# Kernel optimization log

Measured on AMD Instinct MI355X. Metric: run time of the kernel, lower is better.

Reference implementation:

```python
import jax, jax.numpy as jnp
import numpy as np

N, T = 128, 256
QN, QD = 16, 32           # Qn_num, Qn_dim
QL_SIZES = [100] * 8      # Ql category sizes
LD = 32                   # Ql_dim
H = 1024                  # hidden_dim
L = 2                     # layer_num
OUT = 2                   # output_dim
IN_DIM = QN * QD + len(QL_SIZES) * LD  # 768
EPS = 1e-5


def setup_inputs() -> dict:
    key = jax.random.key(0)
    ks = jax.random.split(key, 14)
    qn = jax.random.normal(ks[0], (N, T, QN), dtype=jnp.float32)
    ql = jax.random.randint(ks[1], (N, T, len(QL_SIZES)), 0, 100).astype(jnp.float32)
    x = jnp.concatenate([qn, ql], axis=2)  # [N,T,24]
    std = 1.0 / np.sqrt(H)
    u = lambda k, s: jax.random.uniform(k, s, minval=-std, maxval=std, dtype=jnp.float32)
    return dict(
        x=x,
        QnV=jax.random.normal(ks[2], (QN, QD), dtype=jnp.float32) * 0.5,
        QlV=jax.random.normal(ks[3], (sum(QL_SIZES), LD), dtype=jnp.float32) * 0.5,
        bn_gamma=jnp.ones((QN,), jnp.float32),
        bn_beta=jnp.zeros((QN,), jnp.float32),
        W0=u(ks[4], (IN_DIM + H, 4 * H)), b0=u(ks[5], (4 * H,)),
        W1=u(ks[6], (2 * H, 4 * H)), b1=u(ks[7], (4 * H,)),
        ln_gamma=u(ks[8], (L, 4, H)), ln_beta=u(ks[9], (L, 4, H)),
        fcW=u(ks[10], (H, OUT)), fcb=u(ks[11], (OUT,)),
    )


def _layernorm(v, g, b):
    m = v.mean(-1, keepdims=True)
    s = v.var(-1, keepdims=True)
    return (v - m) * jax.lax.rsqrt(s + EPS) * g + b


def reference(x, QnV, QlV, bn_gamma, bn_beta, W0, b0, W1, b1, ln_gamma, ln_beta, fcW, fcb):
    # ---- data_trans ----
    qn = x[:, :, :QN]                               # [N,T,QN] float features
    ql_idx = x[:, :, QN:].astype(jnp.int32)         # [N,T,Lq] category indices
    offsets = jnp.asarray(np.concatenate([[0], np.cumsum(QL_SIZES)[:-1]]), jnp.int32)
    ql_idx = ql_idx + offsets.reshape(1, 1, -1)
    # BatchNorm1d (training mode): stats over flattened N*T rows, per feature
    flat = qn.reshape(-1, QN)
    mu = flat.mean(0)
    var = flat.var(0)
    qn = (qn - mu) * jax.lax.rsqrt(var + EPS) * bn_gamma + bn_beta
    qn_emb = qn[..., None] * QnV                    # einsum ijk,kd->ijkd : [N,T,QN,QD]
    ql_emb = QlV[ql_idx]                            # [N,T,Lq,LD]
    feats = jnp.concatenate([qn_emb, ql_emb], axis=2).reshape(N, T, IN_DIM)

    Ws, bs = [W0, W1], [b0, b1]

    def step(carry, xt):  # xt: [N, IN_DIM]
        hn, cn = carry     # each [L, N, H]
        xcur = xt
        hs, cs = [], []
        for i in range(L):
            inp = jnp.concatenate([hn[i], xcur], axis=1)
            gates = inp @ Ws[i] + bs[i]             # [N, 4H]
            ig, fg, gg, og = jnp.split(gates, 4, axis=1)
            ig = jax.nn.sigmoid(_layernorm(ig, ln_gamma[i, 0], ln_beta[i, 0]))
            fg = jax.nn.sigmoid(_layernorm(fg, ln_gamma[i, 1], ln_beta[i, 1]))
            gn = _layernorm(gg, ln_gamma[i, 2], ln_beta[i, 2])
            og = jax.nn.sigmoid(_layernorm(og, ln_gamma[i, 3], ln_beta[i, 3]))
            c = cn[i] * fg + ig * jnp.tanh(gn)
            # NOTE: original adds the pre-tanh normalized cellgate (quirk, kept faithful)
            xcur = og * jnp.tanh(c) + gn
            hs.append(xcur)
            cs.append(c)
        return (jnp.stack(hs), jnp.stack(cs)), xcur  # emit last layer h

    h0 = jnp.zeros((L, N, H), jnp.float32)
    c0 = jnp.zeros((L, N, H), jnp.float32)
    xs = jnp.transpose(feats, (1, 0, 2))            # [T, N, IN_DIM]
    _, outs = jax.lax.scan(step, (h0, c0), xs)      # [T, N, H]
    outs = jnp.transpose(outs, (1, 0, 2))           # [N, T, H]
    logits = outs @ fcW + fcb                       # [N, T, OUT]
    return jax.nn.softmax(logits, axis=2)
```

## Files before the change

kernel.cpp:

```cpp
#include <hip/hip_runtime.h>
#include <math.h>


#define N_   128
#define T_   256
#define QN_  16
#define INX  24
#define H_   1024
#define G4   4096
#define FDIM 768
#define EPS_ 1e-5f
#define K0_  1792
#define K1_  2048
#define NSLOT 8
#define HSZ  ((size_t)N_ * H_)
#define SSLOT 16
#define SLSZ (512 * 16)

typedef unsigned short u16;
typedef unsigned int u32;
typedef unsigned long long u64;
typedef __attribute__((ext_vector_type(8))) short bf16x8;
typedef __attribute__((ext_vector_type(4))) float f32x4;

__device__ __forceinline__ float sigmoidf_(float v) { return 1.0f / (1.0f + expf(-v)); }

__device__ __forceinline__ u16 f2bf(float f) {
  unsigned u = __float_as_uint(f);
  u += 0x7fffu + ((u >> 16) & 1u);
  return (u16)(u >> 16);
}
__device__ __forceinline__ float bf2f(u16 x) {
  return __uint_as_float((u32)x << 16);
}

__device__ __forceinline__ void st_u64g(void* p, u64 v) {
  __hip_atomic_store((u64*)p, v, __ATOMIC_RELAXED, __HIP_MEMORY_SCOPE_AGENT);
}
__device__ __forceinline__ void st_f32g(float* p, float v) {
  __hip_atomic_store(p, v, __ATOMIC_RELAXED, __HIP_MEMORY_SCOPE_AGENT);
}
__device__ __forceinline__ u64 ld_u64g(const void* p) {
  return __hip_atomic_load((const u64*)p, __ATOMIC_RELAXED, __HIP_MEMORY_SCOPE_AGENT);
}
__device__ __forceinline__ void atomAdd_(float* p, float v) {
  __hip_atomic_fetch_add(p, v, __ATOMIC_RELAXED, __HIP_MEMORY_SCOPE_AGENT);
}

__global__ __launch_bounds__(256) void bn_stats_k(const float* __restrict__ x,
    const float* __restrict__ gamma, const float* __restrict__ beta,
    float* __restrict__ scale, float* __restrict__ shift) {
  int q = blockIdx.x;
  int tid = threadIdx.x;
  float s = 0.f, s2 = 0.f;
  for (int r = tid; r < N_ * T_; r += 256) {
    float v = x[(size_t)r * INX + q];
    s += v; s2 += v * v;
  }
  for (int off = 32; off; off >>= 1) { s += __shfl_down(s, off); s2 += __shfl_down(s2, off); }
  __shared__ float red[2][4];
  int w = tid >> 6;
  if ((tid & 63) == 0) { red[0][w] = s; red[1][w] = s2; }
  __syncthreads();
  if (tid == 0) {
    float S = 0.f, S2 = 0.f;
    for (int i = 0; i < 4; ++i) { S += red[0][i]; S2 += red[1][i]; }
    float m   = S  / (float)(N_ * T_);
    float var = S2 / (float)(N_ * T_) - m * m;
    float rs  = rsqrtf(var + EPS_);
    scale[q] = rs * gamma[q];
    shift[q] = beta[q] - m * rs * gamma[q];
  }
}

__global__ __launch_bounds__(256) void feats_all_k(const float* __restrict__ x,
    const float* __restrict__ scale, const float* __restrict__ shift,
    const float* __restrict__ QnV, const float* __restrict__ QlV,
    u16* __restrict__ ft) {
  int rid = blockIdx.x;
  int t = rid >> 7, n = rid & 127;
  const float* xr = x + ((size_t)n * T_ + t) * INX;
  u16* frow = ft + (size_t)rid * FDIM;
  for (int f = threadIdx.x; f < FDIM; f += 256) {
    int d = f & 31;
    float v;
    if (f < 512) {
      int q = f >> 5;
      v = (xr[q] * scale[q] + shift[q]) * QnV[q * 32 + d];
    } else {
      int cg_ = (f - 512) >> 5;
      int idx = (int)xr[QN_ + cg_] + cg_ * 100;
      v = QlV[idx * 32 + d];
    }
    frow[f] = f2bf(v);
  }
}

__global__ __launch_bounds__(256) void wconv_k(const float* __restrict__ W,
                                               u16* __restrict__ WtP, int K) {
  __shared__ u16 L[64][72];
  int tid = threadIdx.x;
  int k0 = blockIdx.x * 64, n0 = blockIdx.y * 64;
#pragma unroll
  for (int it = 0; it < 16; ++it) {
    int e = it * 256 + tid;
    int r = e >> 6, c = e & 63;
    L[r][c] = f2bf(W[(size_t)(k0 + r) * G4 + n0 + c]);
  }
  __syncthreads();
  int n = tid >> 2, ks = (tid & 3) << 4;
  int col = n0 + n;
  int b = (col & 1023) >> 3;
  int j = (col >> 10) * 8 + (col & 7);
  u16* dst = WtP + ((size_t)(b * 32 + j)) * K + k0 + ks;
#pragma unroll
  for (int jj = 0; jj < 16; ++jj) dst[jj] = L[ks + jj][n];
}

__device__ __forceinline__ void arrive_(u32* cnts, int fam, int sub) {
  __hip_atomic_fetch_add(&cnts[(fam * 8 + sub) * 16], 1u,
                         __ATOMIC_RELAXED, __HIP_MEMORY_SCOPE_AGENT);
}
__device__ __forceinline__ void poll_(u32* cnts, int fam, int sub, u32 tgt) {
  while (__hip_atomic_load(&cnts[(fam * 8 + sub) * 16],
                           __ATOMIC_RELAXED, __HIP_MEMORY_SCOPE_AGENT) < tgt)
    __builtin_amdgcn_s_sleep(1);
}
__device__ __forceinline__ void acqf_(int tid) {
  if (tid < 64) __builtin_amdgcn_fence(__ATOMIC_ACQUIRE, "agent");
  __syncthreads();
}

template<int NS>
__device__ __forceinline__ void gpart(f32x4& a0, f32x4& a1,
    const u16* __restrict__ abase, const u16* __restrict__ wb0,
    const u16* __restrict__ wb1, int cb, int swz, int g) {
#pragma unroll 8
  for (int kc = 0; kc < NS; ++kc) {
    bf16x8 av = *(const bf16x8*)(abase + kc * 32);
    int c = ((cb + kc * 4 + g) ^ swz) << 3;
    bf16x8 bv0 = *(const bf16x8*)(wb0 + c);
    bf16x8 bv1 = *(const bf16x8*)(wb1 + c);
    a0 = __builtin_amdgcn_mfma_f32_16x16x32_bf16(av, bv0, a0, 0, 0, 0);
    a1 = __builtin_amdgcn_mfma_f32_16x16x32_bf16(av, bv1, a1, 0, 0, 0);
  }
}

__device__ __forceinline__ float lnrm(float v, u64 sq, float g_, float b_) {
  float s = __uint_as_float((u32)sq);
  float q = __uint_as_float((u32)(sq >> 32));
  float mean = s * (1.f / (float)H_);
  float var  = q * (1.f / (float)H_) - mean * mean;
  return (v - mean) * rsqrtf(var + EPS_) * g_ + b_;
}

__global__ __launch_bounds__(512, 2) void persist_k(
    const u16* __restrict__ WtP0, const u16* __restrict__ WtP1,
    const u16* __restrict__ ft,
    u16* __restrict__ h0s, u16* __restrict__ h1s,
    const float* __restrict__ b0, const float* __restrict__ b1,
    const float* __restrict__ lng, const float* __restrict__ lnb,
    const float* __restrict__ fcW, const float* __restrict__ fcb,
    float* __restrict__ statsA, float* __restrict__ statsB,
    u32* __restrict__ cnts, float* __restrict__ out) {
  __shared__ u16 wlds[32 * K1_];
  const int bcu = blockIdx.x, tid = threadIdx.x;
  const int isL0 = bcu < 128;
  const int b    = isL0 ? bcu : bcu - 128;
  const int wave = tid >> 6, lane = tid & 63;
  const int vcol = lane & 15, g4 = lane >> 4;
  const int ga = vcol >> 3, hh = vcol & 7;
  const int swz = vcol & 7;
  const int rowA  = wave * 16 + vcol;
  const int wbase = wave * 16;
  const int sub   = b >> 4;
  const int hbase = b * 8;
  const int K = isL0 ? K0_ : K1_;

  {
    const u16* wsrc = isL0 ? WtP0 + (size_t)b * 32 * K0_
                           : WtP1 + (size_t)b * 32 * K1_;
    int kc8 = K >> 3;
    for (int cid = tid; cid < 32 * kc8; cid += 512) {
      int j = cid / kc8, ck = cid - j * kc8;
      *(bf16x8*)&wlds[j * K + ((ck ^ (j & 7)) << 3)] =
          *(const bf16x8*)&wsrc[(size_t)j * K + (ck << 3)];
    }
  }
  __syncthreads();
  acqf_(tid);

  const u16* wb0p = &wlds[vcol * K];
  const u16* wb1p = &wlds[(vcol + 16) * K];

  const float* bW   = isL0 ? b0 : b1;
  const float* lngW = isL0 ? lng : lng + 4 * H_;
  const float* lnbW = isL0 ? lnb : lnb + 4 * H_;
  const int colA = ga * H_ + hbase + hh;
  const int colB = (ga + 2) * H_ + hbase + hh;
  const float bias0v = bW[colA], bias1v = bW[colB];
  const float lng0v = lngW[colA], lnb0v = lnbW[colA];
  const float lng1v = lngW[colB], lnb1v = lnbW[colB];
  const float fcb0 = fcb[0], fcb1 = fcb[1];

  float cst[4] = {0.f, 0.f, 0.f, 0.f};

  if (isL0) {
    f32x4 acN0 = {0.f, 0.f, 0.f, 0.f}, acN1 = acN0;
    gpart<24>(acN0, acN1, ft + (size_t)rowA * FDIM + g4 * 8, wb0p, wb1p, 128, swz, g4);

    for (int t = 0; t < T_; ++t) {
      const u32 tgt = (u32)(t + 1) * 16u;
      u16* h0w = h0s + (size_t)(t & (NSLOT - 1)) * HSZ;
      const u16* h0r = h0s + (size_t)((t - 1) & (NSLOT - 1)) * HSZ;
      float* stA = statsA + (size_t)(t & (SSLOT - 1)) * SLSZ;

      f32x4 ac0 = acN0, ac1 = acN1;
      gpart<32>(ac0, ac1, h0r + (size_t)rowA * H_ + g4 * 8, wb0p, wb1p, 0, swz, g4);
      f32x4 accb0, accb1;
#pragma unroll
      for (int r = 0; r < 4; ++r) { accb0[r] = ac0[r] + bias0v; accb1[r] = ac1[r] + bias1v; }

#pragma unroll
      for (int r = 0; r < 4; ++r) {
        int row = wbase + g4 * 4 + r;
        float s0 = accb0[r], q0 = s0 * s0, s1 = accb1[r], q1 = s1 * s1;
#pragma unroll
        for (int off = 1; off <= 4; off <<= 1) {
          s0 += __shfl_xor(s0, off); q0 += __shfl_xor(q0, off);
          s1 += __shfl_xor(s1, off); q1 += __shfl_xor(q1, off);
        }
        if (hh == 0) {
          atomAdd_(&stA[(row * 4 + ga) * 16],     s0);
          atomAdd_(&stA[(row * 4 + ga) * 16 + 1], q0);
          atomAdd_(&stA[(row * 4 + ga + 2) * 16],     s1);
          atomAdd_(&stA[(row * 4 + ga + 2) * 16 + 1], q1);
        }
      }
      asm volatile("s_waitcnt vmcnt(0)" ::: "memory");
      __syncthreads();
      if (tid == 0) arrive_(cnts, 0, sub);

      {
        float* zs = statsA + (size_t)((t + 8) & (SSLOT - 1)) * SLSZ;
        if (tid < 64) st_f32g(&zs[(b * 4 + (tid >> 4)) * 16 + (tid & 15)], 0.f);
        int tn = (t + 1 < T_) ? t + 1 : t;
        acN0[0] = 0.f; acN0[1] = 0.f; acN0[2] = 0.f; acN0[3] = 0.f;
        acN1 = acN0;
        gpart<24>(acN0, acN1, ft + ((size_t)tn * N_ + rowA) * FDIM + g4 * 8,
                  wb0p, wb1p, 128, swz, g4);
      }
      if (tid < 8) poll_(cnts, 0, tid, tgt);
      else if (tid < 16 && t >= 7) poll_(cnts, 2, tid - 8, (u32)(t - 6) * 16u);
      __syncthreads();

      u64 sv0[4], sv1[4];
#pragma unroll
      for (int r = 0; r < 4; ++r) {
        int row = wbase + g4 * 4 + r;
        sv0[r] = ld_u64g(&stA[(row * 4 + ga) * 16]);
        sv1[r] = ld_u64g(&stA[(row * 4 + ga + 2) * 16]);
      }
#pragma unroll
      for (int r = 0; r < 4; ++r) {
        int row = wbase + g4 * 4 + r;
        float nv0 = lnrm(accb0[r], sv0[r], lng0v, lnb0v);
        float nv1 = lnrm(accb1[r], sv1[r], lng1v, lnb1v);
        float o0 = __shfl_xor(nv0, 8), o1 = __shfl_xor(nv1, 8);
        float vi = ga ? o0 : nv0;
        float vf = ga ? nv0 : o0;
        float vg = ga ? o1 : nv1;
        float vo = ga ? nv1 : o1;
        float igt = sigmoidf_(vi), fgt = sigmoidf_(vf), ogt = sigmoidf_(vo);
        float cn = cst[r] * fgt + igt * tanhf(vg);
        float xn = ogt * tanhf(cn) + vg;
        cst[r] = cn;
        u32 xv = f2bf(xn);
        u32 oth = __shfl_xor((int)xv, 1);
        u32 pr = (hh & 1) ? ((oth & 0xffffu) | (xv << 16)) : ((xv & 0xffffu) | (oth << 16));
        u32 p2 = __shfl_xor((int)pr, 2);
        if (ga == 0 && (hh & 3) == 0)
          st_u64g(&h0w[(size_t)row * H_ + hbase + hh], ((u64)p2 << 32) | pr);
      }
      asm volatile("s_waitcnt vmcnt(0)" ::: "memory");
      __syncthreads();
      if (tid == 0) arrive_(cnts, 1, sub);
      if (tid < 8) poll_(cnts, 1, tid, tgt);
      __syncthreads();
      if ((t & (NSLOT - 1)) == NSLOT - 2) acqf_(tid);
    }
  } else {
    for (int t = 0; t < T_; ++t) {
      const u32 tgt = (u32)(t + 1) * 16u;
      const u16* h0r = h0s + (size_t)(t & (NSLOT - 1)) * HSZ;
      u16* h1w = h1s + (size_t)(t & (NSLOT - 1)) * HSZ;
      const u16* h1r = h1s + (size_t)((t - 1) & (NSLOT - 1)) * HSZ;
      float* stA = statsB + (size_t)(t & (SSLOT - 1)) * SLSZ;

      if (t > 0 && wave == 0) {
        const u16* hrow = h1r + (size_t)b * H_;
        int col = lane * 16;
        bf16x8 v0 = *(const bf16x8*)(hrow + col);
        bf16x8 v1 = *(const bf16x8*)(hrow + col + 8);
        float L0v = 0.f, L1v = 0.f;
#pragma unroll
        for (int j = 0; j < 8; ++j) {
          float x0 = bf2f((u16)v0[j]);
          float2 fw = *(const float2*)&fcW[(col + j) * 2];
          L0v = fmaf(x0, fw.x, L0v); L1v = fmaf(x0, fw.y, L1v);
          float x1 = bf2f((u16)v1[j]);
          float2 fw2 = *(const float2*)&fcW[(col + 8 + j) * 2];
          L0v = fmaf(x1, fw2.x, L0v); L1v = fmaf(x1, fw2.y, L1v);
        }
#pragma unroll
        for (int off = 1; off <= 32; off <<= 1) { L0v += __shfl_xor(L0v, off); L1v += __shfl_xor(L1v, off); }
        if (lane == 0) {
          L0v += fcb0; L1v += fcb1;
          float mx = fmaxf(L0v, L1v);
          float e0 = expf(L0v - mx), e1 = expf(L1v - mx);
          float inv = 1.f / (e0 + e1);
          *(float2*)&out[((size_t)b * T_ + (t - 1)) * 2] = make_float2(e0 * inv, e1 * inv);
        }
      }

      f32x4 ac0 = {0.f, 0.f, 0.f, 0.f}, ac1 = ac0;
      gpart<32>(ac0, ac1, h1r + (size_t)rowA * H_ + g4 * 8, wb0p, wb1p, 0, swz, g4);

      if (tid < 8) poll_(cnts, 1, tid, tgt);
      __syncthreads();
      gpart<32>(ac0, ac1, h0r + (size_t)rowA * H_ + g4 * 8, wb0p, wb1p, 128, swz, g4);
      f32x4 accb0, accb1;
#pragma unroll
      for (int r = 0; r < 4; ++r) { accb0[r] = ac0[r] + bias0v; accb1[r] = ac1[r] + bias1v; }

#pragma unroll
      for (int r = 0; r < 4; ++r) {
        int row = wbase + g4 * 4 + r;
        float s0 = accb0[r], q0 = s0 * s0, s1 = accb1[r], q1 = s1 * s1;
#pragma unroll
        for (int off = 1; off <= 4; off <<= 1) {
          s0 += __shfl_xor(s0, off); q0 += __shfl_xor(q0, off);
          s1 += __shfl_xor(s1, off); q1 += __shfl_xor(q1, off);
        }
        if (hh == 0) {
          atomAdd_(&stA[(row * 4 + ga) * 16],     s0);
          atomAdd_(&stA[(row * 4 + ga) * 16 + 1], q0);
          atomAdd_(&stA[(row * 4 + ga + 2) * 16],     s1);
          atomAdd_(&stA[(row * 4 + ga + 2) * 16 + 1], q1);
        }
      }
      asm volatile("s_waitcnt vmcnt(0)" ::: "memory");
      __syncthreads();
      if (tid == 0) arrive_(cnts, 2, sub);
      {
        float* zs = statsB + (size_t)((t + 8) & (SSLOT - 1)) * SLSZ;
        if (tid < 64) st_f32g(&zs[(b * 4 + (tid >> 4)) * 16 + (tid & 15)], 0.f);
      }
      if (tid < 8) poll_(cnts, 2, tid, tgt);
      __syncthreads();

      u64 sv0[4], sv1[4];
#pragma unroll
      for (int r = 0; r < 4; ++r) {
        int row = wbase + g4 * 4 + r;
        sv0[r] = ld_u64g(&stA[(row * 4 + ga) * 16]);
        sv1[r] = ld_u64g(&stA[(row * 4 + ga + 2) * 16]);
      }
#pragma unroll
      for (int r = 0; r < 4; ++r) {
        int row = wbase + g4 * 4 + r;
        float nv0 = lnrm(accb0[r], sv0[r], lng0v, lnb0v);
        float nv1 = lnrm(accb1[r], sv1[r], lng1v, lnb1v);
        float o0 = __shfl_xor(nv0, 8), o1 = __shfl_xor(nv1, 8);
        float vi = ga ? o0 : nv0;
        float vf = ga ? nv0 : o0;
        float vg = ga ? o1 : nv1;
        float vo = ga ? nv1 : o1;
        float igt = sigmoidf_(vi), fgt = sigmoidf_(vf), ogt = sigmoidf_(vo);
        float cn = cst[r] * fgt + igt * tanhf(vg);
        float xn = ogt * tanhf(cn) + vg;
        cst[r] = cn;
        u32 xv = f2bf(xn);
        u32 oth = __shfl_xor((int)xv, 1);
        u32 pr = (hh & 1) ? ((oth & 0xffffu) | (xv << 16)) : ((xv & 0xffffu) | (oth << 16));
        u32 p2 = __shfl_xor((int)pr, 2);
        if (ga == 0 && (hh & 3) == 0)
          st_u64g(&h1w[(size_t)row * H_ + hbase + hh], ((u64)p2 << 32) | pr);
      }
      asm volatile("s_waitcnt vmcnt(0)" ::: "memory");
      __syncthreads();
      if (tid == 0) arrive_(cnts, 3, sub);
      if (tid < 8) poll_(cnts, 3, tid, tgt);
      __syncthreads();
      if ((t & (NSLOT - 1)) == NSLOT - 2) acqf_(tid);
    }
    if (wave == 0) {
      const u16* hrow = h1s + (size_t)((T_ - 1) & (NSLOT - 1)) * HSZ + (size_t)b * H_;
      int col = lane * 16;
      bf16x8 v0 = *(const bf16x8*)(hrow + col);
      bf16x8 v1 = *(const bf16x8*)(hrow + col + 8);
      float L0v = 0.f, L1v = 0.f;
#pragma unroll
      for (int j = 0; j < 8; ++j) {
        float x0 = bf2f((u16)v0[j]);
        float2 fw = *(const float2*)&fcW[(col + j) * 2];
        L0v = fmaf(x0, fw.x, L0v); L1v = fmaf(x0, fw.y, L1v);
        float x1 = bf2f((u16)v1[j]);
        float2 fw2 = *(const float2*)&fcW[(col + 8 + j) * 2];
        L0v = fmaf(x1, fw2.x, L0v); L1v = fmaf(x1, fw2.y, L1v);
      }
#pragma unroll
      for (int off = 1; off <= 32; off <<= 1) { L0v += __shfl_xor(L0v, off); L1v += __shfl_xor(L1v, off); }
      if (lane == 0) {
        L0v += fcb0; L1v += fcb1;
        float mx = fmaxf(L0v, L1v);
        float e0 = expf(L0v - mx), e1 = expf(L1v - mx);
        float inv = 1.f / (e0 + e1);
        *(float2*)&out[((size_t)b * T_ + (T_ - 1)) * 2] = make_float2(e0 * inv, e1 * inv);
      }
    }
  }
}

extern "C" void kernel_launch(void* const* d_in, const int* in_sizes, int n_in,
                              void* d_out, int out_size, void* d_ws, size_t ws_size,
                              hipStream_t stream) {
  const float* x   = (const float*)d_in[0];
  const float* QnV = (const float*)d_in[1];
  const float* QlV = (const float*)d_in[2];
  const float* bng = (const float*)d_in[3];
  const float* bnb = (const float*)d_in[4];
  const float* W0  = (const float*)d_in[5];
  const float* b0  = (const float*)d_in[6];
  const float* W1  = (const float*)d_in[7];
  const float* b1  = (const float*)d_in[8];
  const float* lng = (const float*)d_in[9];
  const float* lnb = (const float*)d_in[10];
  const float* fcW = (const float*)d_in[11];
  const float* fcb = (const float*)d_in[12];
  float* out = (float*)d_out;

  u32*   cnts   = (u32*)d_ws;
  float* statsA = (float*)(cnts + 1024);
  float* statsB = statsA + (size_t)SSLOT * SLSZ;
  u16*   h0s    = (u16*)(statsB + (size_t)SSLOT * SLSZ);
  u16*   h1s    = h0s + (size_t)NSLOT * HSZ;
  size_t zero_bytes = (size_t)((char*)(h1s + (size_t)NSLOT * HSZ) - (char*)d_ws);

  float* scale = (float*)(h1s + (size_t)NSLOT * HSZ);
  float* shift = scale + 64;
  u16* ft   = (u16*)(shift + 64);
  u16* WtP0 = ft + (size_t)N_ * T_ * FDIM;
  u16* WtP1 = WtP0 + (size_t)G4 * K0_;

  hipMemsetAsync(d_ws, 0, zero_bytes, stream);

  bn_stats_k<<<QN_, 256, 0, stream>>>(x, bng, bnb, scale, shift);
  feats_all_k<<<N_ * T_, 256, 0, stream>>>(x, scale, shift, QnV, QlV, ft);
  wconv_k<<<dim3(K0_ / 64, G4 / 64), 256, 0, stream>>>(W0, WtP0, K0_);
  wconv_k<<<dim3(K1_ / 64, G4 / 64), 256, 0, stream>>>(W1, WtP1, K1_);

  void* args[] = {
    (void*)&WtP0, (void*)&WtP1, (void*)&ft, (void*)&h0s, (void*)&h1s,
    (void*)&b0, (void*)&b1, (void*)&lng, (void*)&lnb,
    (void*)&fcW, (void*)&fcb, (void*)&statsA, (void*)&statsB,
    (void*)&cnts, (void*)&out
  };
  hipLaunchCooperativeKernel((void*)persist_k, dim3(256), dim3(512), args, 0, stream);
}
```

Baseline: 10.18 ms.

## Use tree barrier with single flag and bank-split LayerNorm stat atomics

Replaces the per-subgroup counter polling, where 8 threads each spin on a counter, with a two-level tree barrier. The last arriver at each subgroup counter bumps a top counter, and the last of those publishes a single flag that one thread polls. LayerNorm partial sums are spread across 8 bank slots per row/gate to reduce atomic contention on the same address, then each block sums the 8 banks into shared memory before normalising. This adds an extra reduction pass, an extra __syncthreads and a larger stats buffer, and the tree adds serial atomic latency on the critical path.

```diff
diff --git a/kernel.cpp b/kernel.cpp
--- a/kernel.cpp
+++ b/kernel.cpp
@@ -15,7 +15,7 @@
 #define NSLOT 8
 #define HSZ  ((size_t)N_ * H_)
 #define SSLOT 16
-#define SLSZ (512 * 16)
+#define SLSZ (512 * 8 * 16)
 
 typedef unsigned short u16;
 typedef unsigned int u32;
@@ -117,13 +117,22 @@
   for (int jj = 0; jj < 16; ++jj) dst[jj] = L[ks + jj][n];
 }
 
-__device__ __forceinline__ void arrive_(u32* cnts, int fam, int sub) {
-  __hip_atomic_fetch_add(&cnts[(fam * 8 + sub) * 16], 1u,
-                         __ATOMIC_RELAXED, __HIP_MEMORY_SCOPE_AGENT);
-}
-__device__ __forceinline__ void poll_(u32* cnts, int fam, int sub, u32 tgt) {
-  while (__hip_atomic_load(&cnts[(fam * 8 + sub) * 16],
-                           __ATOMIC_RELAXED, __HIP_MEMORY_SCOPE_AGENT) < tgt)
+#define SUBC(fam, sub) cnts[((fam) * 8 + (sub)) * 16]
+#define TOPC(fam)      cnts[(32 + (fam)) * 16]
+#define FLAGC(fam)     cnts[(40 + (fam)) * 16]
+
+__device__ __forceinline__ void arrive_tree_(u32* cnts, int fam, int sub, u32 t1) {
+  u32 old = __hip_atomic_fetch_add(&SUBC(fam, sub), 1u,
+                                   __ATOMIC_RELAXED, __HIP_MEMORY_SCOPE_AGENT);
+  if (old == t1 * 16u - 1u) {
+    u32 ot = __hip_atomic_fetch_add(&TOPC(fam), 1u,
+                                    __ATOMIC_RELAXED, __HIP_MEMORY_SCOPE_AGENT);
+    if (ot == t1 * 8u - 1u)
+      __hip_atomic_store(&FLAGC(fam), t1, __ATOMIC_RELAXED, __HIP_MEMORY_SCOPE_AGENT);
+  }
+}
+__device__ __forceinline__ void pollflag_(u32* cnts, int fam, u32 t1) {
+  while (__hip_atomic_load(&FLAGC(fam), __ATOMIC_RELAXED, __HIP_MEMORY_SCOPE_AGENT) < t1)
     __builtin_amdgcn_s_sleep(1);
 }
 __device__ __forceinline__ void acqf_(int tid) {
@@ -146,11 +155,9 @@
   }
 }
 
-__device__ __forceinline__ float lnrm(float v, u64 sq, float g_, float b_) {
-  float s = __uint_as_float((u32)sq);
-  float q = __uint_as_float((u32)(sq >> 32));
-  float mean = s * (1.f / (float)H_);
-  float var  = q * (1.f / (float)H_) - mean * mean;
+__device__ __forceinline__ float lnrm2(float v, float2 sq, float g_, float b_) {
+  float mean = sq.x * (1.f / (float)H_);
+  float var  = sq.y * (1.f / (float)H_) - mean * mean;
   return (v - mean) * rsqrtf(var + EPS_) * g_ + b_;
 }
 
@@ -164,6 +171,7 @@
     float* __restrict__ statsA, float* __restrict__ statsB,
     u32* __restrict__ cnts, float* __restrict__ out) {
   __shared__ u16 wlds[32 * K1_];
+  __shared__ float2 sstat[512];
   const int bcu = blockIdx.x, tid = threadIdx.x;
   const int isL0 = bcu < 128;
   const int b    = isL0 ? bcu : bcu - 128;
@@ -174,6 +182,7 @@
   const int rowA  = wave * 16 + vcol;
   const int wbase = wave * 16;
   const int sub   = b >> 4;
+  const int bank  = b & 7;
   const int hbase = b * 8;
   const int K = isL0 ? K0_ : K1_;
 
@@ -210,7 +219,7 @@
     gpart<24>(acN0, acN1, ft + (size_t)rowA * FDIM + g4 * 8, wb0p, wb1p, 128, swz, g4);
 
     for (int t = 0; t < T_; ++t) {
-      const u32 tgt = (u32)(t + 1) * 16u;
+      const u32 t1 = (u32)(t + 1);
       u16* h0w = h0s + (size_t)(t & (NSLOT - 1)) * HSZ;
       const u16* h0r = h0s + (size_t)((t - 1) & (NSLOT - 1)) * HSZ;
       float* stA = statsA + (size_t)(t & (SSLOT - 1)) * SLSZ;
@@ -231,41 +240,51 @@
           s1 += __shfl_xor(s1, off); q1 += __shfl_xor(q1, off);
         }
         if (hh == 0) {
-          atomAdd_(&stA[(row * 4 + ga) * 16],     s0);
-          atomAdd_(&stA[(row * 4 + ga) * 16 + 1], q0);
-          atomAdd_(&stA[(row * 4 + ga + 2) * 16],     s1);
-          atomAdd_(&stA[(row * 4 + ga + 2) * 16 + 1], q1);
+          float* l0 = &stA[(((row * 4 + ga) * 8) + bank) * 16];
+          float* l1 = &stA[(((row * 4 + ga + 2) * 8) + bank) * 16];
+          atomAdd_(l0, s0);     atomAdd_(l0 + 1, q0);
+          atomAdd_(l1, s1);     atomAdd_(l1 + 1, q1);
         }
       }
       asm volatile("s_waitcnt vmcnt(0)" ::: "memory");
       __syncthreads();
-      if (tid == 0) arrive_(cnts, 0, sub);
+      if (tid == 0) arrive_tree_(cnts, 0, sub, t1);
 
       {
         float* zs = statsA + (size_t)((t + 8) & (SSLOT - 1)) * SLSZ;
-        if (tid < 64) st_f32g(&zs[(b * 4 + (tid >> 4)) * 16 + (tid & 15)], 0.f);
+        if (tid < 64) st_f32g(&zs[(b * 32 + (tid >> 1)) * 16 + (tid & 1)], 0.f);
         int tn = (t + 1 < T_) ? t + 1 : t;
         acN0[0] = 0.f; acN0[1] = 0.f; acN0[2] = 0.f; acN0[3] = 0.f;
         acN1 = acN0;
         gpart<24>(acN0, acN1, ft + ((size_t)tn * N_ + rowA) * FDIM + g4 * 8,
                   wb0p, wb1p, 128, swz, g4);
       }
-      if (tid < 8) poll_(cnts, 0, tid, tgt);
-      else if (tid < 16 && t >= 7) poll_(cnts, 2, tid - 8, (u32)(t - 6) * 16u);
-      __syncthreads();
-
-      u64 sv0[4], sv1[4];
+      if (tid == 0) {
+        pollflag_(cnts, 0, t1);
+        if (t >= 7) pollflag_(cnts, 2, (u32)(t - 6));
+      }
+      __syncthreads();
+
+      {
+        const float* lp = &stA[(size_t)tid * 128];
+        float s = 0.f, q = 0.f;
+#pragma unroll
+        for (int k = 0; k < 8; ++k) {
+          u64 v = ld_u64g(lp + k * 16);
+          s += __uint_as_float((u32)v);
+          q += __uint_as_float((u32)(v >> 32));
+        }
+        sstat[tid] = make_float2(s, q);
+      }
+      __syncthreads();
+
 #pragma unroll
       for (int r = 0; r < 4; ++r) {
         int row = wbase + g4 * 4 + r;
-        sv0[r] = ld_u64g(&stA[(row * 4 + ga) * 16]);
-        sv1[r] = ld_u64g(&stA[(row * 4 + ga + 2) * 16]);
-      }
-#pragma unroll
-      for (int r = 0; r < 4; ++r) {
-        int row = wbase + g4 * 4 + r;
-        float nv0 = lnrm(accb0[r], sv0[r], lng0v, lnb0v);
-        float nv1 = lnrm(accb1[r], sv1[r], lng1v, lnb1v);
+        float2 sv0 = sstat[row * 4 + ga];
+        float2 sv1 = sstat[row * 4 + ga + 2];
+        float nv0 = lnrm2(accb0[r], sv0, lng0v, lnb0v);
+        float nv1 = lnrm2(accb1[r], sv1, lng1v, lnb1v);
         float o0 = __shfl_xor(nv0, 8), o1 = __shfl_xor(nv1, 8);
         float vi = ga ? o0 : nv0;
         float vf = ga ? nv0 : o0;
@@ -284,14 +303,13 @@
       }
       asm volatile("s_waitcnt vmcnt(0)" ::: "memory");
       __syncthreads();
-      if (tid == 0) arrive_(cnts, 1, sub);
-      if (tid < 8) poll_(cnts, 1, tid, tgt);
+      if (tid == 0) { arrive_tree_(cnts, 1, sub, t1); pollflag_(cnts, 1, t1); }
       __syncthreads();
       if ((t & (NSLOT - 1)) == NSLOT - 2) acqf_(tid);
     }
   } else {
     for (int t = 0; t < T_; ++t) {
-      const u32 tgt = (u32)(t + 1) * 16u;
+      const u32 t1 = (u32)(t + 1);
       const u16* h0r = h0s + (size_t)(t & (NSLOT - 1)) * HSZ;
       u16* h1w = h1s + (size_t)(t & (NSLOT - 1)) * HSZ;
       const u16* h1r = h1s + (size_t)((t - 1) & (NSLOT - 1)) * HSZ;
@@ -326,7 +344,7 @@
       f32x4 ac0 = {0.f, 0.f, 0.f, 0.f}, ac1 = ac0;
       gpart<32>(ac0, ac1, h1r + (size_t)rowA * H_ + g4 * 8, wb0p, wb1p, 0, swz, g4);
 
-      if (tid < 8) poll_(cnts, 1, tid, tgt);
+      if (tid == 0) pollflag_(cnts, 1, t1);
       __syncthreads();
       gpart<32>(ac0, ac1, h0r + (size_t)rowA * H_ + g4 * 8, wb0p, wb1p, 128, swz, g4);
       f32x4 accb0, accb1;
@@ -343,34 +361,42 @@
           s1 += __shfl_xor(s1, off); q1 += __shfl_xor(q1, off);
         }
         if (hh == 0) {
-          atomAdd_(&stA[(row * 4 + ga) * 16],     s0);
-          atomAdd_(&stA[(row * 4 + ga) * 16 + 1], q0);
-          atomAdd_(&stA[(row * 4 + ga + 2) * 16],     s1);
-          atomAdd_(&stA[(row * 4 + ga + 2) * 16 + 1], q1);
+          float* l0 = &stA[(((row * 4 + ga) * 8) + bank) * 16];
+          float* l1 = &stA[(((row * 4 + ga + 2) * 8) + bank) * 16];
+          atomAdd_(l0, s0);     atomAdd_(l0 + 1, q0);
+          atomAdd_(l1, s1);     atomAdd_(l1 + 1, q1);
         }
       }
       asm volatile("s_waitcnt vmcnt(0)" ::: "memory");
       __syncthreads();
-      if (tid == 0) arrive_(cnts, 2, sub);
+      if (tid == 0) arrive_tree_(cnts, 2, sub, t1);
       {
         float* zs = statsB + (size_t)((t + 8) & (SSLOT - 1)) * SLSZ;
-        if (tid < 64) st_f32g(&zs[(b * 4 + (tid >> 4)) * 16 + (tid & 15)], 0.f);
-      }
-      if (tid < 8) poll_(cnts, 2, tid, tgt);
-      __syncthreads();
-
-      u64 sv0[4], sv1[4];
+        if (tid < 64) st_f32g(&zs[(b * 32 + (tid >> 1)) * 16 + (tid & 1)], 0.f);
+      }
+      if (tid == 0) pollflag_(cnts, 2, t1);
+      __syncthreads();
+
+      {
+        const float* lp = &stA[(size_t)tid * 128];
+        float s = 0.f, q = 0.f;
+#pragma unroll
+        for (int k = 0; k < 8; ++k) {
+          u64 v = ld_u64g(lp + k * 16);
+          s += __uint_as_float((u32)v);
+          q += __uint_as_float((u32)(v >> 32));
+        }
+        sstat[tid] = make_float2(s, q);
+      }
+      __syncthreads();
+
 #pragma unroll
       for (int r = 0; r < 4; ++r) {
         int row = wbase + g4 * 4 + r;
-        sv0[r] = ld_u64g(&stA[(row * 4 + ga) * 16]);
-        sv1[r] = ld_u64g(&stA[(row * 4 + ga + 2) * 16]);
-      }
-#pragma unroll
-      for (int r = 0; r < 4; ++r) {
-        int row = wbase + g4 * 4 + r;
-        float nv0 = lnrm(accb0[r], sv0[r], lng0v, lnb0v);
-        float nv1 = lnrm(accb1[r], sv1[r], lng1v, lnb1v);
+        float2 sv0 = sstat[row * 4 + ga];
+        float2 sv1 = sstat[row * 4 + ga + 2];
+        float nv0 = lnrm2(accb0[r], sv0, lng0v, lnb0v);
+        float nv1 = lnrm2(accb1[r], sv1, lng1v, lnb1v);
         float o0 = __shfl_xor(nv0, 8), o1 = __shfl_xor(nv1, 8);
         float vi = ga ? o0 : nv0;
         float vf = ga ? nv0 : o0;
@@ -389,8 +415,7 @@
       }
       asm volatile("s_waitcnt vmcnt(0)" ::: "memory");
       __syncthreads();
-      if (tid == 0) arrive_(cnts, 3, sub);
-      if (tid < 8) poll_(cnts, 3, tid, tgt);
+      if (tid == 0) { arrive_tree_(cnts, 3, sub, t1); pollflag_(cnts, 3, t1); }
       __syncthreads();
       if ((t & (NSLOT - 1)) == NSLOT - 2) acqf_(tid);
     }
```

Result: faster. 8.967 ms (-12.0%).
